# Performance work log

Measured on AMD Instinct MI355X. Metric: run time of the kernel, lower is better.

## Reference

```python
import jax, jax.numpy as jnp
import numpy as np

D_MODEL, D_STATE, EXPAND = 256, 16, 2
D_INNER = EXPAND * D_MODEL
DT_RANK = (D_MODEL + 15) // 16
BATCH, SEQLEN = 4, 4096


def silu(x):
    return x * jax.nn.sigmoid(x)


def setup_inputs() -> dict:
    key = jax.random.key(0)
    ks = jax.random.split(key, 10)
    h = jax.random.normal(ks[0], (BATCH, SEQLEN, D_MODEL), dtype=jnp.float32)
    Wi_f = jax.random.normal(ks[1], (2 * D_INNER, D_MODEL), dtype=jnp.float32) / np.sqrt(D_MODEL)
    Wi_b = jax.random.normal(ks[2], (2 * D_INNER, D_MODEL), dtype=jnp.float32) / np.sqrt(D_MODEL)
    Wx_f = jax.random.normal(ks[3], (DT_RANK + 2 * D_STATE, D_INNER), dtype=jnp.float32) / np.sqrt(D_INNER)
    Wx_b = jax.random.normal(ks[4], (DT_RANK + 2 * D_STATE, D_INNER), dtype=jnp.float32) / np.sqrt(D_INNER)
    dt_std = DT_RANK ** -0.5
    Wdt_f = jax.random.uniform(ks[5], (D_INNER, DT_RANK), dtype=jnp.float32, minval=-dt_std, maxval=dt_std)
    Wdt_b = jax.random.uniform(ks[6], (D_INNER, DT_RANK), dtype=jnp.float32, minval=-dt_std, maxval=dt_std)
    # dt bias = inverse-softplus of dt sampled log-uniform in [1e-3, 1e-1]
    dt = jnp.exp(jax.random.uniform(ks[7], (D_INNER,), dtype=jnp.float32) * (np.log(0.1) - np.log(0.001)) + np.log(0.001))
    dt = jnp.clip(dt, 1e-4, None)
    inv_dt = dt + jnp.log(-jnp.expm1(-dt))
    bdt_f = inv_dt
    bdt_b = inv_dt
    A_log = jnp.log(jnp.broadcast_to(jnp.arange(1, D_STATE + 1, dtype=jnp.float32), (D_INNER, D_STATE)))
    A_log_f = A_log
    A_log_b = A_log
    D_f = jnp.ones((D_INNER,), dtype=jnp.float32)
    D_b = jnp.ones((D_INNER,), dtype=jnp.float32)
    Wo = jax.random.normal(ks[8], (D_MODEL, 2 * D_INNER), dtype=jnp.float32) / np.sqrt(2 * D_INNER)
    return {"hidden_states": h, "Wi_f": Wi_f, "Wi_b": Wi_b, "Wx_f": Wx_f, "Wx_b": Wx_b,
            "Wdt_f": Wdt_f, "Wdt_b": Wdt_b, "bdt_f": bdt_f, "bdt_b": bdt_b,
            "A_log_f": A_log_f, "A_log_b": A_log_b, "D_f": D_f, "D_b": D_b, "Wo": Wo}


def mamba_dir(h, Wi, Wx, Wdt, bdt, A_log, Dp, reverse):
    b, l, _ = h.shape
    di, r = Wdt.shape
    n = A_log.shape[1]
    xz = h @ Wi.T                      # [b,l,2*di]
    if reverse:
        xz = xz[:, ::-1]
    x, z = xz[..., :di], xz[..., di:]
    u = silu(x)                        # selective_scan input u
    x_dbl = u @ Wx.T                   # [b,l,r+2n]
    delta = jax.nn.softplus(x_dbl[..., :r] @ Wdt.T + bdt)   # [b,l,di]
    Bm = x_dbl[..., r:r + n]           # [b,l,n]
    Cm = x_dbl[..., r + n:r + 2 * n]   # [b,l,n]
    A = -jnp.exp(A_log)                # [di,n]

    def step(s, inp):
        u_t, d_t, B_t, C_t = inp       # [b,di],[b,di],[b,n],[b,n]
        dA = jnp.exp(d_t[..., None] * A)                         # [b,di,n]
        s = dA * s + (d_t * u_t)[..., None] * B_t[:, None, :]    # [b,di,n]
        y_t = jnp.einsum('bdn,bn->bd', s, C_t)
        return s, y_t

    s0 = jnp.zeros((b, di, n), dtype=u.dtype)
    xs = (jnp.swapaxes(u, 0, 1), jnp.swapaxes(delta, 0, 1),
          jnp.swapaxes(Bm, 0, 1), jnp.swapaxes(Cm, 0, 1))
    _, ys = jax.lax.scan(step, s0, xs)
    y = jnp.swapaxes(ys, 0, 1) + u * Dp          # skip term D*u
    y = y * silu(z)                              # gated output
    if reverse:
        y = y[:, ::-1]
    return y


def reference(hidden_states, Wi_f, Wi_b, Wx_f, Wx_b, Wdt_f, Wdt_b, bdt_f, bdt_b, A_log_f, A_log_b, D_f, D_b, Wo):
    y_f = mamba_dir(hidden_states, Wi_f, Wx_f, Wdt_f, bdt_f, A_log_f, D_f, False)
    y_b = mamba_dir(hidden_states, Wi_b, Wx_b, Wdt_b, bdt_b, A_log_b, D_b, True)
    y = jnp.concatenate([y_f, y_b], axis=-1)     # [b,l,2*di]
    return y @ Wo.T                              # [b,l,d_model]
```

## Files before the change

kernel.cpp:

```cpp
#include <hip/hip_runtime.h>
#include <hip/hip_bf16.h>
#include <cstddef>
#include <cstdint>

#define D_MODELc 256
#define D_STATEc 16
#define D_INNERc 512
#define DT_RANKc 16
#define BATCHc   4
#define SEQLENc  4096
#define NCHUNK   128
#define CHUNK    32

typedef unsigned short u16;
typedef __attribute__((ext_vector_type(8))) short bf16x8;
typedef __attribute__((ext_vector_type(4))) float f32x4;
typedef float __attribute__((ext_vector_type(4))) f4v;

#define VMCNT8() asm volatile("s_waitcnt vmcnt(8)" ::: "memory")
#define VMCNT0() asm volatile("s_waitcnt vmcnt(0)" ::: "memory")

__device__ __forceinline__ float siluf(float v) { return v / (1.f + __expf(-v)); }

__device__ __forceinline__ u16 bf16_rne(float f) {
    uint32_t u = __float_as_uint(f);
    u += 0x7fffu + ((u >> 16) & 1u);
    return (u16)(u >> 16);
}
__device__ __forceinline__ float bf16_to_f(u16 h) {
    return __uint_as_float(((uint32_t)h) << 16);
}
__device__ __forceinline__ uint32_t pack_hl(float f) {
    u16 hh = bf16_rne(f);
    u16 ll = bf16_rne(f - bf16_to_f(hh));
    return ((uint32_t)hh << 16) | ll;
}
__device__ __forceinline__ float unpack_add(uint32_t v) {
    return __uint_as_float(v & 0xFFFF0000u) + __uint_as_float(v << 16);
}
__device__ __forceinline__ void unpack_frag(const uint32_t* q, bf16x8& fh, bf16x8& fl) {
    union { bf16x8 v; uint32_t w[4]; } H, L;
    #pragma unroll
    for (int i = 0; i < 4; i++) {
        uint32_t a = q[2 * i], b = q[2 * i + 1];
        H.w[i] = (a >> 16) | (b & 0xFFFF0000u);
        L.w[i] = (a & 0xFFFFu) | (b << 16);
    }
    fh = H.v; fl = L.v;
}
__device__ __forceinline__ float softplusf(float x) {
    return fmaxf(x, 0.f) + __logf(1.f + __expf(-fabsf(x)));
}
__device__ __forceinline__ float dot16_tree(const f4v x[4], const float* w, float bias) {
    float t0 = fmaf(x[0][1], w[1],  x[0][0] * w[0]);
    float t1 = fmaf(x[0][3], w[3],  x[0][2] * w[2]);
    float t2 = fmaf(x[1][1], w[5],  x[1][0] * w[4]);
    float t3 = fmaf(x[1][3], w[7],  x[1][2] * w[6]);
    float t4 = fmaf(x[2][1], w[9],  x[2][0] * w[8]);
    float t5 = fmaf(x[2][3], w[11], x[2][2] * w[10]);
    float t6 = fmaf(x[3][1], w[13], x[3][0] * w[12]);
    float t7 = fmaf(x[3][3], w[15], x[3][2] * w[14]);
    return bias + (((t0 + t1) + (t2 + t3)) + ((t4 + t5) + (t6 + t7)));
}
__device__ __forceinline__ void qladder(float q, float* qd) {
    float q2 = q * q;
    float q4 = q2 * q2;
    float q8 = q4 * q4;
    qd[0] = q;        qd[1] = q2;       qd[2] = q2 * q;     qd[3] = q4;
    qd[4] = q4 * q;   qd[5] = q4 * q2;  qd[6] = q4 * qd[2]; qd[7] = q8;
    qd[8] = q8 * q;   qd[9] = q8 * q2;  qd[10] = q8 * qd[2]; qd[11] = q8 * q4;
    qd[12] = q8 * qd[4]; qd[13] = q8 * qd[5]; qd[14] = q8 * qd[6]; qd[15] = q8 * q8;
}

#define GLL16(g, l) __builtin_amdgcn_global_load_lds( \
    (const __attribute__((address_space(1))) uint32_t*)(g), \
    (__attribute__((address_space(3))) uint32_t*)(l), 16, 0, 0)

__global__ __launch_bounds__(256) void split5_kernel(
        const float* __restrict__ s0, const float* __restrict__ s1,
        const float* __restrict__ s2, const float* __restrict__ s3,
        const float* __restrict__ s4,
        u16* __restrict__ h0, u16* __restrict__ l0,
        u16* __restrict__ h1, u16* __restrict__ l1,
        u16* __restrict__ h2, u16* __restrict__ l2,
        u16* __restrict__ h3, u16* __restrict__ l3,
        u16* __restrict__ h4, u16* __restrict__ l4,
        int n4w, int n4x) {
    const int which = blockIdx.y;
    const float* in; u16* hi; u16* lo; int n4;
    if      (which == 0) { in = s0; hi = h0; lo = l0; n4 = n4w; }
    else if (which == 1) { in = s1; hi = h1; lo = l1; n4 = n4w; }
    else if (which == 2) { in = s2; hi = h2; lo = l2; n4 = n4w; }
    else if (which == 3) { in = s3; hi = h3; lo = l3; n4 = n4x; }
    else                 { in = s4; hi = h4; lo = l4; n4 = n4x; }
    for (int i = blockIdx.x * 256 + threadIdx.x; i < n4; i += gridDim.x * 256) {
        float4 v = ((const float4*)in)[i];
        u16 a0 = bf16_rne(v.x), a1 = bf16_rne(v.y), a2 = bf16_rne(v.z), a3 = bf16_rne(v.w);
        ushort4 hv; hv.x = a0; hv.y = a1; hv.z = a2; hv.w = a3;
        ushort4 lv;
        lv.x = bf16_rne(v.x - bf16_to_f(a0));
        lv.y = bf16_rne(v.y - bf16_to_f(a1));
        lv.z = bf16_rne(v.z - bf16_to_f(a2));
        lv.w = bf16_rne(v.w - bf16_to_f(a3));
        ((ushort4*)hi)[i] = hv;
        ((ushort4*)lo)[i] = lv;
    }
}

__global__ __launch_bounds__(256) void split_kernel(const float* __restrict__ in,
                                                    u16* __restrict__ hi,
                                                    u16* __restrict__ lo, int n4) {
    int i = blockIdx.x * 256 + threadIdx.x;
    const int stride = gridDim.x * 256;
    for (; i < n4; i += stride) {
        float4 v = ((const float4*)in)[i];
        u16 a0 = bf16_rne(v.x), a1 = bf16_rne(v.y), a2 = bf16_rne(v.z), a3 = bf16_rne(v.w);
        ushort4 hv; hv.x = a0; hv.y = a1; hv.z = a2; hv.w = a3;
        ushort4 lv;
        lv.x = bf16_rne(v.x - bf16_to_f(a0));
        lv.y = bf16_rne(v.y - bf16_to_f(a1));
        lv.z = bf16_rne(v.z - bf16_to_f(a2));
        lv.w = bf16_rne(v.w - bf16_to_f(a3));
        ((ushort4*)hi)[i] = hv;
        ((ushort4*)lo)[i] = lv;
    }
}

template<int EPI, int NBL2, int AINT>
__global__ __launch_bounds__(256) void gemm_mfma(
        const u16* __restrict__ Ah, const u16* __restrict__ Al, int lda,
        const u16* __restrict__ Bh, const u16* __restrict__ Bl, int ldb,
        float* __restrict__ out0,
        uint32_t* __restrict__ uhl,
        int M, int N, int K) {
    __shared__ char lds[2][32768];
    const int t    = threadIdx.x;
    const int lane = t & 63;
    const int wid  = t >> 6;
    const int wrow = wid >> 1, wcol = wid & 1;

    const int id  = blockIdx.x;
    const int xcd = id & 7;
    const int j   = id >> 3;
    const int nb  = j & ((1 << NBL2) - 1);
    const int mg  = j >> NBL2;
    const int m0  = (mg * 8 + xcd) * 128;
    const int n0  = nb * 128;

    const int lr  = lane & 15;
    const int kgl = lane >> 4;

    f32x4 acc[4][4] = {};

    const char* gp[8];
    if (AINT == 0) {
        #pragma unroll
        for (int i = 0; i < 8; i++) {
            int c    = i * 256 + t;
            int tile = c >> 9;
            int kg   = (c >> 7) & 3;
            int row  = c & 127;
            const u16* bsrc = (tile == 0) ? Ah : (tile == 1) ? Al : (tile == 2) ? Bh : Bl;
            int r0 = (tile < 2) ? m0 : n0;
            int ld = (tile < 2) ? lda : ldb;
            gp[i] = (const char*)(bsrc + (size_t)(r0 + row) * ld + kg * 8);
        }
    } else {
        #pragma unroll
        for (int i = 0; i < 4; i++) {
            int c    = i * 256 + t;
            int kg   = c >> 8;
            int row  = (c >> 1) & 127;
            int half = c & 1;
            gp[i] = (const char*)((const uint32_t*)Ah + (size_t)(m0 + row) * lda + kg * 8 + half * 4);
        }
        #pragma unroll
        for (int i = 4; i < 8; i++) {
            int cb   = (i - 4) * 256 + t;
            int tile = cb >> 9;
            int kg   = (cb >> 7) & 3;
            int row  = cb & 127;
            const u16* bsrc = tile ? Bl : Bh;
            gp[i] = (const char*)(bsrc + (size_t)(n0 + row) * ldb + kg * 8);
        }
    }
    const int ldst_t = t << 4;

    auto stage = [&](int buf) {
        #pragma unroll
        for (int i = 0; i < 8; i++) {
            GLL16(gp[i], ((char*)lds) + buf * 32768 + i * 4096 + ldst_t);
            gp[i] += (AINT == 1 && i < 4) ? 128 : 64;
        }
    };

    const int NT = K >> 5;
    stage(0);
    if (NT > 1) stage(1);

    for (int kt = 0; kt < NT; ++kt) {
        const int buf = kt & 1;
        if (kt + 1 < NT) { VMCNT8(); } else { VMCNT0(); }
        __builtin_amdgcn_sched_barrier(0);
        __builtin_amdgcn_s_barrier();
        __builtin_amdgcn_sched_barrier(0);

        bf16x8 afh[4], afl[4];
        if (AINT == 0) {
            const u16* lb = (const u16*)lds[buf];
            #pragma unroll
            for (int mi = 0; mi < 4; mi++) {
                int row = wrow * 64 + mi * 16 + lr;
                afh[mi] = *(const bf16x8*)(lb + 0 * 4096 + kgl * 1024 + row * 8);
                afl[mi] = *(const bf16x8*)(lb + 1 * 4096 + kgl * 1024 + row * 8);
            }
        } else {
            const uint32_t* la = (const uint32_t*)lds[buf];
            #pragma unroll
            for (int mi = 0; mi < 4; mi++) {
                int row = wrow * 64 + mi * 16 + lr;
                unpack_frag(la + kgl * 1024 + row * 8, afh[mi], afl[mi]);
            }
        }
        const u16* lbB = (const u16*)(lds[buf] + 16384);
        #pragma unroll
        for (int ni = 0; ni < 4; ni++) {
            int row = wcol * 64 + ni * 16 + lr;
            bf16x8 bfh = *(const bf16x8*)(lbB + 0 * 4096 + kgl * 1024 + row * 8);
            bf16x8 bfl = *(const bf16x8*)(lbB + 1 * 4096 + kgl * 1024 + row * 8);
            #pragma unroll
            for (int mi = 0; mi < 4; mi++) {
                acc[mi][ni] = __builtin_amdgcn_mfma_f32_16x16x32_bf16(afh[mi], bfh, acc[mi][ni], 0, 0, 0);
                acc[mi][ni] = __builtin_amdgcn_mfma_f32_16x16x32_bf16(afh[mi], bfl, acc[mi][ni], 0, 0, 0);
                acc[mi][ni] = __builtin_amdgcn_mfma_f32_16x16x32_bf16(afl[mi], bfh, acc[mi][ni], 0, 0, 0);
            }
        }
        __builtin_amdgcn_sched_barrier(0);
        __builtin_amdgcn_s_barrier();
        __builtin_amdgcn_sched_barrier(0);
        if (kt + 2 < NT) stage(buf);
    }

    #pragma unroll
    for (int mi = 0; mi < 4; mi++) {
        #pragma unroll
        for (int ni = 0; ni < 4; ni++) {
            #pragma unroll
            for (int r = 0; r < 4; r++) {
                int m = m0 + wrow * 64 + mi * 16 + kgl * 4 + r;
                int n = n0 + wcol * 64 + ni * 16 + lr;
                float v = acc[mi][ni][r];
                if (EPI == 0) {
                    __builtin_nontemporal_store(v, &out0[(size_t)m * N + n]);
                } else {
                    float s = siluf(v);
                    int dirn = n >> 10;
                    int nn   = n & 1023;
                    if (nn < 512) {
                        size_t dof = (size_t)dirn * (size_t)M * 512;
                        uhl[dof + (size_t)m * 512 + nn] = pack_hl(s);
                    } else {
                        out0[(size_t)m * 1024 + dirn * 512 + (nn - 512)] = s;
                    }
                }
            }
        }
    }
}

__global__ __launch_bounds__(256) void xdbl_mfma(
        const uint32_t* __restrict__ Uhl,
        const u16* __restrict__ WxH, const u16* __restrict__ WxL,
        float* __restrict__ out) {
    __shared__ uint32_t lds[4][64][8];
    const int t    = threadIdx.x;
    const int lane = t & 63;
    const int wid  = t >> 6;
    const int m0   = blockIdx.x * 64;
    const int dir  = blockIdx.y;
    const int Mp   = gridDim.x * 64;
    const int lr   = lane & 15;
    const int kgl  = lane >> 4;

    const size_t dofU = (size_t)dir * (size_t)Mp * 512;
    const size_t dofW = (size_t)dir * (size_t)48 * 512;

    const char* gp[2];
    #pragma unroll
    for (int i = 0; i < 2; i++) {
        int c    = i * 256 + t;
        int kg   = c >> 7;
        int row  = (c >> 1) & 63;
        int half = c & 1;
        gp[i] = (const char*)(Uhl + dofU + (size_t)(m0 + row) * 512 + kg * 8 + half * 4);
    }
    const int ldst_t = t << 4;

    f32x4 acc[3] = {};

    for (int k0 = 0; k0 < 512; k0 += 32) {
        #pragma unroll
        for (int i = 0; i < 2; i++) {
            GLL16(gp[i], ((char*)lds) + i * 4096 + ldst_t);
            gp[i] += 128;
        }
        __syncthreads();

        bf16x8 afh, afl;
        unpack_frag(&lds[kgl][wid * 16 + lr][0], afh, afl);
        #pragma unroll
        for (int nf = 0; nf < 3; nf++) {
            const size_t boff = dofW + (size_t)(nf * 16 + lr) * 512 + k0 + kgl * 8;
            bf16x8 bfh = *(const bf16x8*)(WxH + boff);
            bf16x8 bfl = *(const bf16x8*)(WxL + boff);
            acc[nf] = __builtin_amdgcn_mfma_f32_16x16x32_bf16(afh, bfh, acc[nf], 0, 0, 0);
            acc[nf] = __builtin_amdgcn_mfma_f32_16x16x32_bf16(afh, bfl, acc[nf], 0, 0, 0);
            acc[nf] = __builtin_amdgcn_mfma_f32_16x16x32_bf16(afl, bfh, acc[nf], 0, 0, 0);
        }
        __syncthreads();
    }

    float* o = out + (size_t)dir * (size_t)Mp * 48;
    #pragma unroll
    for (int nf = 0; nf < 3; nf++) {
        #pragma unroll
        for (int r = 0; r < 4; r++) {
            int m = m0 + wid * 16 + kgl * 4 + r;
            int n = nf * 16 + lr;
            o[(size_t)m * 48 + n] = acc[nf][r];
        }
    }
}

__global__ __launch_bounds__(256) void scan_phaseA(
        const uint32_t* __restrict__ Uhl,
        const float* __restrict__ XD,
        const float* __restrict__ Wdt_f, const float* __restrict__ Wdt_b,
        const float* __restrict__ bdt_f, const float* __restrict__ bdt_b,
        const float* __restrict__ AL_f, const float* __restrict__ AL_b,
        float* __restrict__ SDL, float* __restrict__ S) {
    const int c   = blockIdx.x;
    const int d   = blockIdx.y * 256 + threadIdx.x;
    const int z   = blockIdx.z;
    const int dir = z & 1;
    const int b   = z >> 1;
    const int PB  = gridDim.z >> 1;
    const int Mp  = PB * SEQLENc;
    const float* Wdt = dir ? Wdt_b : Wdt_f;
    const float* bdt = dir ? bdt_b : bdt_f;
    const float* AL  = dir ? AL_b  : AL_f;
    const uint32_t* UD = Uhl + (size_t)dir * Mp * 512;
    const float* XDD = XD + (size_t)dir * Mp * 48;

    float w[16], a[16], s[16];
    #pragma unroll
    for (int n = 0; n < 16; n++) {
        w[n] = Wdt[d * 16 + n];
        a[n] = -__expf(AL[d * 16 + n]);
        s[n] = 0.f;
    }
    const float a0 = a[0];
    bool pw = (a0 != 0.f);
    #pragma unroll
    for (int n = 1; n < 16; n++)
        pw = pw && (fabsf(a[n] - (float)(n + 1) * a0) <= 3e-6f * fabsf(a[n]));
    const float bb = bdt[d];
    float sdl = 0.f;

    for (int i = 0; i < CHUNK; i++) {
        int tt = c * CHUNK + i;
        int l  = dir ? (SEQLENc - 1 - tt) : tt;
        size_t row = (size_t)b * SEQLENc + l;
        float uu = unpack_add(UD[row * 512 + d]);
        const f4v* xr4 = (const f4v*)&XDD[row * 48];
        f4v xw[4] = {xr4[0], xr4[1], xr4[2], xr4[3]};
        float dl = softplusf(dot16_tree(xw, w, bb));
        sdl += dl;
        float du = dl * uu;
        if (pw) {
            float qd[16];
            qladder(__expf(a0 * dl), qd);
            #pragma unroll
            for (int g = 0; g < 4; g++) {
                f4v B4 = xr4[4 + g];
                #pragma unroll
                for (int jj = 0; jj < 4; jj++) {
                    int n = g * 4 + jj;
                    s[n] = fmaf(qd[n], s[n], du * B4[jj]);
                }
            }
        } else {
            #pragma unroll
            for (int g = 0; g < 4; g++) {
                f4v B4 = xr4[4 + g];
                #pragma unroll
                for (int jj = 0; jj < 4; jj++) {
                    int n = g * 4 + jj;
                    float dA = __expf(dl * a[n]);
                    s[n] = fmaf(dA, s[n], du * B4[jj]);
                }
            }
        }
    }
    SDL[((size_t)z * NCHUNK + c) * 512 + d] = sdl;
    size_t base = (((size_t)z * NCHUNK + c) * 16) * 512 + d;
    #pragma unroll
    for (int n = 0; n < 16; n++)
        S[base + (size_t)n * 512] = s[n];
}

__global__ __launch_bounds__(256) void scan_phaseB(const float* __restrict__ SDL,
                                                   float* __restrict__ S,
                                                   const float* __restrict__ AL_f,
                                                   const float* __restrict__ AL_b) {
    const int g   = blockIdx.x * 256 + threadIdx.x;
    const int d   = g & 511;
    const int n   = (g >> 9) & 15;
    const int z   = g >> 13;
    const int dir = z & 1;
    const float an = -__expf((dir ? AL_b : AL_f)[d * 16 + n]);
    const size_t strideS = (size_t)16 * 512;
    size_t offS = (((size_t)z * NCHUNK) * 16 + n) * 512 + d;
    size_t offD = ((size_t)z * NCHUNK) * 512 + d;
    float carry = 0.f;
    float sdl = SDL[offD], ss = S[offS];
    for (int c = 0; c < NCHUNK; c++) {
        float sdn = 0.f, sn = 0.f;
        if (c + 1 < NCHUNK) { sdn = SDL[offD + 512]; sn = S[offS + strideS]; }
        float pp = __expf(an * sdl);
        S[offS] = carry;
        carry = pp * carry + ss;
        sdl = sdn; ss = sn;
        offS += strideS; offD += 512;
    }
}

__global__ __launch_bounds__(256) void scan_phaseC(
        const uint32_t* __restrict__ Uhl,
        const float* __restrict__ XD,
        const float* __restrict__ Wdt_f, const float* __restrict__ Wdt_b,
        const float* __restrict__ bdt_f, const float* __restrict__ bdt_b,
        const float* __restrict__ AL_f, const float* __restrict__ AL_b,
        const float* __restrict__ E,
        const float* SZ,
        const float* __restrict__ D_f,  const float* __restrict__ D_b,
        uint32_t* Yhl) {
    const int c   = blockIdx.x;
    const int d   = blockIdx.y * 256 + threadIdx.x;
    const int z   = blockIdx.z;
    const int dir = z & 1;
    const int b   = z >> 1;
    const int PB  = gridDim.z >> 1;
    const int Mp  = PB * SEQLENc;
    const float* Wdt = dir ? Wdt_b : Wdt_f;
    const float* bdt = dir ? bdt_b : bdt_f;
    const float* AL  = dir ? AL_b  : AL_f;
    const uint32_t* UD = Uhl + (size_t)dir * Mp * 512;
    const float* XDD = XD + (size_t)dir * Mp * 48;

    float w[16], a[16], s[16];
    size_t base = (((size_t)z * NCHUNK + c) * 16) * 512 + d;
    #pragma unroll
    for (int n = 0; n < 16; n++) {
        w[n] = Wdt[d * 16 + n];
        a[n] = -__expf(AL[d * 16 + n]);
        s[n] = E[base + (size_t)n * 512];
    }
    const float a0 = a[0];
    bool pw = (a0 != 0.f);
    #pragma unroll
    for (int n = 1; n < 16; n++)
        pw = pw && (fabsf(a[n] - (float)(n + 1) * a0) <= 3e-6f * fabsf(a[n]));
    const float bb = bdt[d];
    const float Dd = (dir ? D_b : D_f)[d];

    for (int i = 0; i < CHUNK; i++) {
        int tt = c * CHUNK + i;
        int l  = dir ? (SEQLENc - 1 - tt) : tt;
        size_t row = (size_t)b * SEQLENc + l;
        float uu = unpack_add(UD[row * 512 + d]);
        const f4v* xr4 = (const f4v*)&XDD[row * 48];
        f4v xw[4] = {xr4[0], xr4[1], xr4[2], xr4[3]};
        float dl = softplusf(dot16_tree(xw, w, bb));
        float du = dl * uu;
        float yp0 = 0.f, yp1 = 0.f, yp2 = 0.f, yp3 = 0.f;
        if (pw) {
            float qd[16];
            qladder(__expf(a0 * dl), qd);
            #pragma unroll
            for (int g = 0; g < 4; g++) {
                f4v B4 = xr4[4 + g];
                f4v C4 = xr4[8 + g];
                float yp = 0.f;
                #pragma unroll
                for (int jj = 0; jj < 4; jj++) {
                    int n = g * 4 + jj;
                    s[n] = fmaf(qd[n], s[n], du * B4[jj]);
                    yp = fmaf(s[n], C4[jj], yp);
                }
                if (g == 0) yp0 = yp; else if (g == 1) yp1 = yp;
                else if (g == 2) yp2 = yp; else yp3 = yp;
            }
        } else {
            #pragma unroll
            for (int g = 0; g < 4; g++) {
                f4v B4 = xr4[4 + g];
                f4v C4 = xr4[8 + g];
                float yp = 0.f;
                #pragma unroll
                for (int jj = 0; jj < 4; jj++) {
                    int n = g * 4 + jj;
                    float dA = __expf(dl * a[n]);
                    s[n] = fmaf(dA, s[n], du * B4[jj]);
                    yp = fmaf(s[n], C4[jj], yp);
                }
                if (g == 0) yp0 = yp; else if (g == 1) yp1 = yp;
                else if (g == 2) yp2 = yp; else yp3 = yp;
            }
        }
        float y = (yp0 + yp1) + (yp2 + yp3);
        size_t zi = row * 1024 + (size_t)dir * 512 + d;
        float sz = SZ[zi];
        float yv = (y + uu * Dd) * sz;
        Yhl[zi] = pack_hl(yv);
    }
}

extern "C" void kernel_launch(void* const* d_in, const int* in_sizes, int n_in,
                              void* d_out, int out_size, void* d_ws, size_t ws_size,
                              hipStream_t stream) {
    const float* h    = (const float*)d_in[0];
    const float* Wi_f = (const float*)d_in[1];
    const float* Wi_b = (const float*)d_in[2];
    const float* Wx_f = (const float*)d_in[3];
    const float* Wx_b = (const float*)d_in[4];
    const float* Wdt_f= (const float*)d_in[5];
    const float* Wdt_b= (const float*)d_in[6];
    const float* bdt_f= (const float*)d_in[7];
    const float* bdt_b= (const float*)d_in[8];
    const float* Al_f = (const float*)d_in[9];
    const float* Al_b = (const float*)d_in[10];
    const float* D_f  = (const float*)d_in[11];
    const float* D_b  = (const float*)d_in[12];
    const float* Wo   = (const float*)d_in[13];
    float* out = (float*)d_out;

    const size_t W_ELE  = 1024 * 256;
    const size_t WX_ELE = 48 * 512;
    const size_t FB   = (size_t)SEQLENc * D_INNERc;
    const size_t FH   = (size_t)SEQLENc * D_MODELc;
    const size_t FX   = (size_t)SEQLENc * 48;
    const size_t FP   = (size_t)NCHUNK * 16 * 512;
    const size_t FD   = (size_t)NCHUNK * 512;

    const size_t fixed_bytes = (8 * W_ELE + 4 * WX_ELE) * sizeof(u16);
    const size_t per_b = 2 * FH * sizeof(u16)
                       + 2 * FB * sizeof(float)
                       + 2 * FB * sizeof(uint32_t)
                       + 2 * FX * sizeof(float)
                       + 2 * (FP + FD) * sizeof(float);
    int PB = 4;
    if (fixed_bytes + 4 * per_b + 65536 > ws_size) PB = 2;
    if (fixed_bytes + 2 * per_b + 65536 > ws_size) PB = 1;

    char* cur = (char*)d_ws;
    auto alloc = [&](size_t bytes) -> char* {
        char* p = cur; cur += (bytes + 255) & ~(size_t)255; return p;
    };
    u16* WiH = (u16*)alloc(2 * W_ELE * 2);
    u16* WiL = (u16*)alloc(2 * W_ELE * 2);
    u16* WoH = (u16*)alloc(W_ELE * 2);
    u16* WoL = (u16*)alloc(W_ELE * 2);
    u16* WxH = (u16*)alloc(2 * WX_ELE * 2);
    u16* WxL = (u16*)alloc(2 * WX_ELE * 2);
    u16*      hH  = (u16*)alloc((size_t)PB * FH * 2);
    u16*      hL  = (u16*)alloc((size_t)PB * FH * 2);
    float*    sz  = (float*)alloc((size_t)PB * 2 * FB * 4);
    uint32_t* uhl = (uint32_t*)alloc((size_t)PB * 2 * FB * 4);
    float*    xd  = (float*)alloc((size_t)PB * 2 * FX * 4);
    float*    SDL = (float*)alloc((size_t)PB * 2 * FD * 4);
    float*    S   = (float*)alloc((size_t)PB * 2 * FP * 4);
    uint32_t* yhl = (uint32_t*)sz;

    {
        int n4w = (int)(W_ELE / 4);
        int n4x = (int)(WX_ELE / 4);
        split5_kernel<<<dim3(64, 5), 256, 0, stream>>>(
            Wi_f, Wi_b, Wo, Wx_f, Wx_b,
            WiH, WiL, WiH + W_ELE, WiL + W_ELE, WoH, WoL,
            WxH, WxL, WxH + WX_ELE, WxL + WX_ELE,
            n4w, n4x);
    }

    for (int b0 = 0; b0 < BATCHc; b0 += PB) {
        const int Mp = PB * SEQLENc;
        const int MB = Mp / 128;
        const float* hB = h   + (size_t)b0 * FH;
        float*       oB = out + (size_t)b0 * FH;

        {
            int n4 = (int)((size_t)PB * FH / 4);
            int blocks = (n4 + 255) / 256; if (blocks > 2048) blocks = 2048;
            split_kernel<<<blocks, 256, 0, stream>>>(hB, hH, hL, n4);
        }

        gemm_mfma<1, 4, 0><<<16 * MB, 256, 0, stream>>>(
            hH, hL, D_MODELc, WiH, WiL, D_MODELc,
            sz, uhl, Mp, 2048, D_MODELc);

        xdbl_mfma<<<dim3(Mp / 64, 2), 256, 0, stream>>>(uhl, WxH, WxL, xd);

        scan_phaseA<<<dim3(NCHUNK, 2, 2 * PB), 256, 0, stream>>>(
            uhl, xd, Wdt_f, Wdt_b, bdt_f, bdt_b, Al_f, Al_b, SDL, S);
        scan_phaseB<<<PB * 64, 256, 0, stream>>>(SDL, S, Al_f, Al_b);
        scan_phaseC<<<dim3(NCHUNK, 2, 2 * PB), 256, 0, stream>>>(
            uhl, xd, Wdt_f, Wdt_b, bdt_f, bdt_b, Al_f, Al_b,
            S, sz, D_f, D_b, yhl);

        gemm_mfma<0, 1, 1><<<2 * MB, 256, 0, stream>>>(
            (const u16*)yhl, nullptr, 1024, WoH, WoL, 1024,
            oB, nullptr, Mp, D_MODELc, 1024);
    }
}
```

Measured before the change: 326.8 us.

## Halve GEMM N-tile to 64 and stage epilogue through LDS for coalesced stores

Shrinks the MFMA GEMM output tile from 128x128 to 128x64, which doubles the number of blocks and cuts LDS use to 48KB, so more blocks can run at once. The epilogue now writes accumulators into padded LDS in two row halves and then issues 16-byte vectorized global stores instead of scattered per-element stores. The trade-off is less reuse of the A tile per block, since the A operand is reloaded for twice as many blocks, plus extra barriers in the epilogue.

After: 352.5 us. 7.9% more time.

```diff
diff --git a/kernel.cpp b/kernel.cpp
--- a/kernel.cpp
+++ b/kernel.cpp
@@ -16,8 +16,9 @@
 typedef __attribute__((ext_vector_type(8))) short bf16x8;
 typedef __attribute__((ext_vector_type(4))) float f32x4;
 typedef float __attribute__((ext_vector_type(4))) f4v;
-
-#define VMCNT8() asm volatile("s_waitcnt vmcnt(8)" ::: "memory")
+typedef __attribute__((ext_vector_type(4))) uint32_t u32x4;
+
+#define VMCNT6() asm volatile("s_waitcnt vmcnt(6)" ::: "memory")
 #define VMCNT0() asm volatile("s_waitcnt vmcnt(0)" ::: "memory")
 
 __device__ __forceinline__ float siluf(float v) { return v / (1.f + __expf(-v)); }
@@ -133,7 +134,7 @@
         float* __restrict__ out0,
         uint32_t* __restrict__ uhl,
         int M, int N, int K) {
-    __shared__ char lds[2][32768];
+    __shared__ char lds[49152];
     const int t    = threadIdx.x;
     const int lane = t & 63;
     const int wid  = t >> 6;
@@ -145,25 +146,23 @@
     const int nb  = j & ((1 << NBL2) - 1);
     const int mg  = j >> NBL2;
     const int m0  = (mg * 8 + xcd) * 128;
-    const int n0  = nb * 128;
+    const int n0  = nb * 64;
 
     const int lr  = lane & 15;
     const int kgl = lane >> 4;
 
-    f32x4 acc[4][4] = {};
-
-    const char* gp[8];
+    f32x4 acc[4][2] = {};
+
+    const char* gp[6];
     if (AINT == 0) {
         #pragma unroll
-        for (int i = 0; i < 8; i++) {
+        for (int i = 0; i < 4; i++) {
             int c    = i * 256 + t;
             int tile = c >> 9;
             int kg   = (c >> 7) & 3;
             int row  = c & 127;
-            const u16* bsrc = (tile == 0) ? Ah : (tile == 1) ? Al : (tile == 2) ? Bh : Bl;
-            int r0 = (tile < 2) ? m0 : n0;
-            int ld = (tile < 2) ? lda : ldb;
-            gp[i] = (const char*)(bsrc + (size_t)(r0 + row) * ld + kg * 8);
+            const u16* bsrc = tile ? Al : Ah;
+            gp[i] = (const char*)(bsrc + (size_t)(m0 + row) * lda + kg * 8);
         }
     } else {
         #pragma unroll
@@ -174,22 +173,22 @@
             int half = c & 1;
             gp[i] = (const char*)((const uint32_t*)Ah + (size_t)(m0 + row) * lda + kg * 8 + half * 4);
         }
-        #pragma unroll
-        for (int i = 4; i < 8; i++) {
-            int cb   = (i - 4) * 256 + t;
-            int tile = cb >> 9;
-            int kg   = (cb >> 7) & 3;
-            int row  = cb & 127;
-            const u16* bsrc = tile ? Bl : Bh;
-            gp[i] = (const char*)(bsrc + (size_t)(n0 + row) * ldb + kg * 8);
-        }
+    }
+    #pragma unroll
+    for (int i = 4; i < 6; i++) {
+        int cb   = (i - 4) * 256 + t;
+        int tile = cb >> 8;
+        int kg   = (cb >> 6) & 3;
+        int row  = cb & 63;
+        const u16* bsrc = tile ? Bl : Bh;
+        gp[i] = (const char*)(bsrc + (size_t)(n0 + row) * ldb + kg * 8);
     }
     const int ldst_t = t << 4;
 
     auto stage = [&](int buf) {
         #pragma unroll
-        for (int i = 0; i < 8; i++) {
-            GLL16(gp[i], ((char*)lds) + buf * 32768 + i * 4096 + ldst_t);
+        for (int i = 0; i < 6; i++) {
+            GLL16(gp[i], ((char*)lds) + buf * 24576 + i * 4096 + ldst_t);
             gp[i] += (AINT == 1 && i < 4) ? 128 : 64;
         }
     };
@@ -200,34 +199,35 @@
 
     for (int kt = 0; kt < NT; ++kt) {
         const int buf = kt & 1;
-        if (kt + 1 < NT) { VMCNT8(); } else { VMCNT0(); }
+        if (kt + 1 < NT) { VMCNT6(); } else { VMCNT0(); }
         __builtin_amdgcn_sched_barrier(0);
         __builtin_amdgcn_s_barrier();
         __builtin_amdgcn_sched_barrier(0);
 
+        const char* lb = lds + buf * 24576;
         bf16x8 afh[4], afl[4];
         if (AINT == 0) {
-            const u16* lb = (const u16*)lds[buf];
+            const u16* lbA = (const u16*)lb;
             #pragma unroll
             for (int mi = 0; mi < 4; mi++) {
                 int row = wrow * 64 + mi * 16 + lr;
-                afh[mi] = *(const bf16x8*)(lb + 0 * 4096 + kgl * 1024 + row * 8);
-                afl[mi] = *(const bf16x8*)(lb + 1 * 4096 + kgl * 1024 + row * 8);
+                afh[mi] = *(const bf16x8*)(lbA + kgl * 1024 + row * 8);
+                afl[mi] = *(const bf16x8*)(lbA + 4096 + kgl * 1024 + row * 8);
             }
         } else {
-            const uint32_t* la = (const uint32_t*)lds[buf];
+            const uint32_t* la = (const uint32_t*)lb;
             #pragma unroll
             for (int mi = 0; mi < 4; mi++) {
                 int row = wrow * 64 + mi * 16 + lr;
                 unpack_frag(la + kgl * 1024 + row * 8, afh[mi], afl[mi]);
             }
         }
-        const u16* lbB = (const u16*)(lds[buf] + 16384);
-        #pragma unroll
-        for (int ni = 0; ni < 4; ni++) {
-            int row = wcol * 64 + ni * 16 + lr;
-            bf16x8 bfh = *(const bf16x8*)(lbB + 0 * 4096 + kgl * 1024 + row * 8);
-            bf16x8 bfl = *(const bf16x8*)(lbB + 1 * 4096 + kgl * 1024 + row * 8);
+        const u16* lbB = (const u16*)(lb + 16384);
+        #pragma unroll
+        for (int ni = 0; ni < 2; ni++) {
+            int col = wcol * 32 + ni * 16 + lr;
+            bf16x8 bfh = *(const bf16x8*)(lbB + kgl * 512 + col * 8);
+            bf16x8 bfl = *(const bf16x8*)(lbB + 2048 + kgl * 512 + col * 8);
             #pragma unroll
             for (int mi = 0; mi < 4; mi++) {
                 acc[mi][ni] = __builtin_amdgcn_mfma_f32_16x16x32_bf16(afh[mi], bfh, acc[mi][ni], 0, 0, 0);
@@ -241,28 +241,49 @@
         if (kt + 2 < NT) stage(buf);
     }
 
-    #pragma unroll
-    for (int mi = 0; mi < 4; mi++) {
-        #pragma unroll
-        for (int ni = 0; ni < 4; ni++) {
-            #pragma unroll
-            for (int r = 0; r < 4; r++) {
-                int m = m0 + wrow * 64 + mi * 16 + kgl * 4 + r;
-                int n = n0 + wcol * 64 + ni * 16 + lr;
-                float v = acc[mi][ni][r];
-                if (EPI == 0) {
-                    __builtin_nontemporal_store(v, &out0[(size_t)m * N + n]);
-                } else {
-                    float s = siluf(v);
-                    int dirn = n >> 10;
-                    int nn   = n & 1023;
-                    if (nn < 512) {
-                        size_t dof = (size_t)dirn * (size_t)M * 512;
-                        uhl[dof + (size_t)m * 512 + nn] = pack_hl(s);
-                    } else {
-                        out0[(size_t)m * 1024 + dirn * 512 + (nn - 512)] = s;
+    uint32_t* lds32 = (uint32_t*)lds;
+    const int dirn = (EPI == 1) ? (nb >> 4) : 0;
+    const bool is_u = (EPI == 1) && ((nb & 15) < 8);
+    const int colbase = (EPI == 1) ? (nb & 7) * 64 : 0;
+    #pragma unroll
+    for (int p = 0; p < 2; p++) {
+        if (p == 1) __syncthreads();
+        if (wrow == p) {
+            #pragma unroll
+            for (int mi = 0; mi < 4; mi++) {
+                #pragma unroll
+                for (int ni = 0; ni < 2; ni++) {
+                    #pragma unroll
+                    for (int r = 0; r < 4; r++) {
+                        int row = mi * 16 + kgl * 4 + r;
+                        int col = wcol * 32 + ni * 16 + lr;
+                        float v = acc[mi][ni][r];
+                        uint32_t w;
+                        if (EPI == 0) w = __float_as_uint(v);
+                        else {
+                            float s = siluf(v);
+                            w = is_u ? pack_hl(s) : __float_as_uint(s);
+                        }
+                        lds32[row * 66 + col] = w;
                     }
                 }
+            }
+        }
+        __syncthreads();
+        #pragma unroll
+        for (int i = 0; i < 4; i++) {
+            int idx = i * 256 + t;
+            int row = idx >> 4, c4 = idx & 15;
+            int gm  = m0 + p * 64 + row;
+            if (EPI == 0) {
+                f4v v = *(const f4v*)(lds32 + row * 66 + c4 * 4);
+                __builtin_nontemporal_store(v, (f4v*)(out0 + (size_t)gm * N + n0 + c4 * 4));
+            } else if (is_u) {
+                *(u32x4*)(uhl + (size_t)dirn * M * 512 + (size_t)gm * 512 + colbase + c4 * 4) =
+                    *(const u32x4*)(lds32 + row * 66 + c4 * 4);
+            } else {
+                *(f4v*)(out0 + (size_t)gm * 1024 + (size_t)dirn * 512 + colbase + c4 * 4) =
+                    *(const f4v*)(lds32 + row * 66 + c4 * 4);
             }
         }
     }
@@ -604,7 +625,7 @@
             split_kernel<<<blocks, 256, 0, stream>>>(hB, hH, hL, n4);
         }
 
-        gemm_mfma<1, 4, 0><<<16 * MB, 256, 0, stream>>>(
+        gemm_mfma<1, 5, 0><<<32 * MB, 256, 0, stream>>>(
             hH, hL, D_MODELc, WiH, WiL, D_MODELc,
             sz, uhl, Mp, 2048, D_MODELc);
 
@@ -617,7 +638,7 @@
             uhl, xd, Wdt_f, Wdt_b, bdt_f, bdt_b, Al_f, Al_b,
             S, sz, D_f, D_b, yhl);
 
-        gemm_mfma<0, 1, 1><<<2 * MB, 256, 0, stream>>>(
+        gemm_mfma<0, 2, 1><<<4 * MB, 256, 0, stream>>>(
             (const u16*)yhl, nullptr, 1024, WoH, WoL, 1024,
             oB, nullptr, Mp, D_MODELc, 1024);
     }
```
